# Optimization experiments

Measured on AMD Instinct MI355X. Metric: run time of the kernel, lower is better.

## Reference

```python
import jax, jax.numpy as jnp
import numpy as np

D = 300      # embedding / model dim
H = 150      # LSTM hidden per direction (dim // 2)
V = 21257    # vocab size
B, S = 1024, 256


def _lstm_run(x, lengths, Wih, Whh, b):
    """Unidirectional masked LSTM. x: [B,S,Din]; outputs [B,S,H].
    State frozen and output zeroed at t >= lengths (packed-sequence semantics)."""
    Bb, Ss, _ = x.shape
    h0 = jnp.zeros((Bb, H), x.dtype)
    c0 = jnp.zeros((Bb, H), x.dtype)

    def step(carry, inp):
        h, c = carry
        xt, t = inp
        g = xt @ Wih.T + h @ Whh.T + b          # [B, 4H]
        i, f, gg, o = jnp.split(g, 4, axis=-1)   # torch gate order i,f,g,o
        i = jax.nn.sigmoid(i); f = jax.nn.sigmoid(f)
        gg = jnp.tanh(gg); o = jax.nn.sigmoid(o)
        c_new = f * c + i * gg
        h_new = o * jnp.tanh(c_new)
        valid = (t < lengths)[:, None]
        h2 = jnp.where(valid, h_new, h)
        c2 = jnp.where(valid, c_new, c)
        return (h2, c2), jnp.where(valid, h_new, jnp.zeros_like(h_new))

    _, ys = jax.lax.scan(step, (h0, c0), (jnp.swapaxes(x, 0, 1), jnp.arange(Ss)))
    return jnp.swapaxes(ys, 0, 1)


def _reverse_valid(x, lengths):
    """Reverse the valid prefix of each sequence; self-inverse on valid region."""
    Ss = x.shape[1]
    t = jnp.arange(Ss)[None, :]
    L = lengths[:, None]
    idx = jnp.where(t < L, L - 1 - t, t)
    return jnp.take_along_axis(x, idx[:, :, None], axis=1)


def _bilstm(x, lengths, pf, pb):
    hf = _lstm_run(x, lengths, *pf)
    hb = _reverse_valid(_lstm_run(_reverse_valid(x, lengths), lengths, *pb), lengths)
    return jnp.concatenate([hf, hb], axis=-1)  # [B,S,2H]


def setup_inputs() -> dict:
    key = jax.random.key(0)
    ks = jax.random.split(key, 20)
    x = jax.random.randint(ks[0], (B, S), 0, V)
    lengths = jax.random.randint(ks[1], (B,), 1, S + 1)
    mask = (jnp.arange(S)[None, :] < lengths[:, None]).astype(jnp.int64)

    def p(k, shape):
        return jax.random.normal(k, shape, dtype=jnp.float32) * 0.05

    emb = p(ks[2], (V, D))
    inp = {"x": x, "mask": mask, "emb": emb}
    # layer 0: input D; layer 1: input 2H (=D)
    names = [("l0f", D), ("l0b", D), ("l1f", 2 * H), ("l1b", 2 * H)]
    ki = 3
    for nm, din in names:
        inp[f"Wih_{nm}"] = p(ks[ki], (4 * H, din)); ki += 1
        inp[f"Whh_{nm}"] = p(ks[ki], (4 * H, H)); ki += 1
        inp[f"b_{nm}"] = p(ks[ki], (4 * H,)); ki += 1
    inp["W1"] = p(ks[15], (D, D)); inp["b1"] = p(ks[16], (D,))
    inp["W2"] = p(ks[17], (D, D)); inp["b2"] = p(ks[18], (D,))
    return inp


def reference(x, mask, emb,
              Wih_l0f, Whh_l0f, b_l0f, Wih_l0b, Whh_l0b, b_l0b,
              Wih_l1f, Whh_l1f, b_l1f, Wih_l1b, Whh_l1b, b_l1b,
              W1, b1, W2, b2):
    lengths = jnp.sum(mask != 0, axis=1)
    emb_z = emb.at[0].set(0.0)                 # padding_idx=0
    xe = emb_z[x]                              # [B,S,D]
    h1 = _bilstm(xe, lengths, (Wih_l0f, Whh_l0f, b_l0f), (Wih_l0b, Whh_l0b, b_l0b))
    h2 = _bilstm(h1, lengths, (Wih_l1f, Whh_l1f, b_l1f), (Wih_l1b, Whh_l1b, b_l1b))
    # gather output at last valid timestep (fwd last step || bwd first step)
    last = jnp.take_along_axis(h2, (lengths - 1)[:, None, None], axis=1)[:, 0, :]  # [B,300]
    # dropout is identity in eval mode
    out = jnp.tanh(last @ W1.T + b1)
    out = out @ W2.T + b2
    return out
```

## Files before the change

kernel.cpp:

```cpp
#include <hip/hip_runtime.h>

typedef unsigned short u16;
typedef __bf16 bf16x8 __attribute__((ext_vector_type(8)));
typedef float f32x4 __attribute__((ext_vector_type(4)));
typedef float f4 __attribute__((ext_vector_type(4)));
typedef unsigned short u16x8 __attribute__((ext_vector_type(8)));
typedef unsigned short u16x4 __attribute__((ext_vector_type(4)));

#define BB 1024
#define SS 256
#define DD 300
#define HH 150
#define GG 600
#define VV 21257
#define VPAD 21376
#define KSTR 320
#define GSTR 600
#define WK 160
#define L2E 1.442695041f
#define L2E2 2.885390082f

static __device__ __forceinline__ float bf2f(u16 u){
  unsigned v = ((unsigned)u) << 16;
  return __builtin_bit_cast(float, v);
}
static __device__ __forceinline__ u16 f2bf(float f){
  unsigned u = __builtin_bit_cast(unsigned, f);
  u = u + 0x7FFFu + ((u >> 16) & 1u);
  return (u16)(u >> 16);
}
static __device__ __forceinline__ float fsig2(float p){
  return __builtin_amdgcn_rcpf(1.0f + __builtin_amdgcn_exp2f(-p));
}
static __device__ __forceinline__ float ftanh2(float p){
  return 2.0f * __builtin_amdgcn_rcpf(1.0f + __builtin_amdgcn_exp2f(-p)) - 1.0f;
}

__global__ void k_len(const int* __restrict__ mask, int* __restrict__ len){
  __shared__ int red[256];
  int b = blockIdx.x, t = threadIdx.x;
  red[t] = (mask[b*SS + t] != 0) ? 1 : 0;
  __syncthreads();
  for (int o = 128; o > 0; o >>= 1){
    if (t < o) red[t] += red[t+o];
    __syncthreads();
  }
  if (t == 0) len[b] = red[0];
}

__global__ void k_sort(const int* __restrict__ len, int* __restrict__ perm){
  __shared__ int L[1024];
  int b = threadIdx.x;
  int l = len[b];
  L[b] = l;
  __syncthreads();
  int r = 0;
  for (int j = 0; j < 1024; ++j){
    int lj = L[j];
    r += (lj < l) || (lj == l && j < b);
  }
  perm[r] = b;
}

struct PrepW {
  const float* src[8];
  u16* dst[8];
  int R[8], C[8], DR[8], DC[8];
};
__global__ void k_prepw(PrepW p){
  int z = blockIdx.y;
  int n = p.DR[z]*p.DC[z];
  for (int i = blockIdx.x*256 + threadIdx.x; i < n; i += 800*256){
    int r = i / p.DC[z], c = i - r*p.DC[z];
    float v = (r < p.R[z] && c < p.C[z]) ? p.src[z][r*p.C[z] + c] : 0.f;
    float sc = (r >= 300 && r < 450) ? L2E2 : L2E;
    p.dst[z][i] = f2bf(v * sc);
  }
}
struct PrepB { const float* src[4]; float* dst[4]; };
__global__ void k_prepb(PrepB p){
  int z = blockIdx.y;
  int i = blockIdx.x*256 + threadIdx.x;
  if (i < 640){
    float v = (i < GG) ? p.src[z][i] : 0.f;
    float sc = (i >= 300 && i < 450) ? L2E2 : L2E;
    p.dst[z][i] = v * sc;
  }
}

__global__ void k_prepemb(const float* __restrict__ emb, u16* __restrict__ dst){
  long i = (long)blockIdx.x*256 + threadIdx.x;
  if (i >= (long)VPAD*KSTR) return;
  int r = (int)(i / KSTR), c = (int)(i - (long)r*KSTR);
  float v = (r >= 1 && r < VV && c < DD) ? emb[(size_t)r*DD + c] : 0.f;
  dst[i] = f2bf(v);
}

__launch_bounds__(512, 2)
__global__ void k_gemm(const u16* __restrict__ A,
                       const u16* __restrict__ Wf, const u16* __restrict__ Wb,
                       const float* __restrict__ bsf, const float* __restrict__ bsb,
                       u16* __restrict__ of, u16* __restrict__ ob)
{
  const u16* W = blockIdx.z ? Wb : Wf;
  const float* bias = blockIdx.z ? bsb : bsf;
  u16* outp = blockIdx.z ? ob : of;

  __shared__ u16 Al[128*40];
  __shared__ u16 Bl[320*40];

  int tid = threadIdx.x;
  int l = tid & 63, w = tid >> 6;
  int lo = l & 15, hi = l >> 4;
  int wm = w >> 2, wn = w & 3;
  int m0 = blockIdx.x * 128;
  int n0 = blockIdx.y * 320;

  int ar = tid >> 2, ac = (tid & 3) * 8;
  const u16* Arow = A + (size_t)(m0 + ar)*KSTR + ac;
  bool bvld[3]; int brr[3], bcc[3];
  const u16* Brow[3];
  #pragma unroll
  for (int i = 0; i < 3; ++i){
    int ch = tid + i*512;
    bvld[i] = (ch < 1280);
    int r2 = bvld[i] ? (ch >> 2) : 0;
    brr[i] = r2; bcc[i] = (ch & 3) * 8;
    Brow[i] = W + (size_t)(n0 + r2)*KSTR + bcc[i];
  }

  u16x8 ra = *(const u16x8*)Arow;
  u16x8 rbv[3];
  #pragma unroll
  for (int i = 0; i < 3; ++i) if (bvld[i]) rbv[i] = *(const u16x8*)Brow[i];

  f32x4 zero = {0.f, 0.f, 0.f, 0.f};
  f32x4 acc[4][5];
  #pragma unroll
  for (int a = 0; a < 4; ++a)
    #pragma unroll
    for (int b = 0; b < 5; ++b) acc[a][b] = zero;

  for (int kk = 0; kk < 10; ++kk){
    __syncthreads();
    *(u16x8*)&Al[ar*40 + ac] = ra;
    #pragma unroll
    for (int i = 0; i < 3; ++i)
      if (bvld[i]) *(u16x8*)&Bl[brr[i]*40 + bcc[i]] = rbv[i];
    __syncthreads();
    if (kk < 9){
      int k1 = (kk+1)*32;
      ra = *(const u16x8*)(Arow + k1);
      #pragma unroll
      for (int i = 0; i < 3; ++i)
        if (bvld[i]) rbv[i] = *(const u16x8*)(Brow[i] + k1);
    }
    u16x8 av[4], bv[5];
    #pragma unroll
    for (int mt = 0; mt < 4; ++mt)
      av[mt] = *(const u16x8*)&Al[(wm*64 + mt*16 + lo)*40 + hi*8];
    #pragma unroll
    for (int nt = 0; nt < 5; ++nt)
      bv[nt] = *(const u16x8*)&Bl[(wn*80 + nt*16 + lo)*40 + hi*8];
    #pragma unroll
    for (int mt = 0; mt < 4; ++mt)
      #pragma unroll
      for (int nt = 0; nt < 5; ++nt)
        acc[mt][nt] = __builtin_amdgcn_mfma_f32_16x16x32_bf16(
            __builtin_bit_cast(bf16x8, av[mt]),
            __builtin_bit_cast(bf16x8, bv[nt]),
            acc[mt][nt], 0, 0, 0);
  }

  #pragma unroll
  for (int mt = 0; mt < 4; ++mt){
    #pragma unroll
    for (int nt = 0; nt < 5; ++nt){
      int col = n0 + wn*80 + nt*16 + lo;
      if (col < GG){
        float bsv = bias[col];
        int g = (col >= 450) ? 3 : (col >= 300) ? 2 : (col >= 150) ? 1 : 0;
        int cofs = (col - g*150)*4 + g;
        #pragma unroll
        for (int r = 0; r < 4; ++r){
          int row = m0 + wm*64 + mt*16 + hi*4 + r;
          outp[(size_t)row*GSTR + cofs] = f2bf(acc[mt][nt][r] + bsv);
        }
      }
    }
  }
}

#define PREF(GB, TT)                                                            \
  {                                                                             \
    _Pragma("unroll")                                                           \
    for (int r = 0; r < 4; ++r){                                                \
      int Li = Lr[r];                                                           \
      int tt = ((TT) < Li) ? (TT) : (Li-1);                                     \
      int s_ = dir ? (Li-1-tt) : tt;                                            \
      int rowi;                                                                 \
      if (isL1) rowi = rowb[r] + s_;                                            \
      else      rowi = (int)tks[(hi*4+r)*256 + s_];                             \
      GB[r] = *(const u16x4*)(xg + (size_t)rowi*GSTR + jjc*4);                  \
    }                                                                           \
  }

#define REC_STEP(T, PB, GB)                                                     \
  {                                                                             \
    f32x4 acc0 = {0,0,0,0}, acc1 = {0,0,0,0}, acc2 = {0,0,0,0}, acc3 = {0,0,0,0}; \
    _Pragma("unroll")                                                           \
    for (int ks = 0; ks < 5; ++ks){                                             \
      u16x8 a_ = *(const u16x8*)&hsm[PB][lo*168 + ks*32 + hi*8];                \
      acc0 = __builtin_amdgcn_mfma_f32_16x16x32_bf16(                           \
          __builtin_bit_cast(bf16x8, a_), __builtin_bit_cast(bf16x8, bw[0][ks]), acc0, 0,0,0); \
      acc1 = __builtin_amdgcn_mfma_f32_16x16x32_bf16(                           \
          __builtin_bit_cast(bf16x8, a_), __builtin_bit_cast(bf16x8, bw[1][ks]), acc1, 0,0,0); \
      acc2 = __builtin_amdgcn_mfma_f32_16x16x32_bf16(                           \
          __builtin_bit_cast(bf16x8, a_), __builtin_bit_cast(bf16x8, bw[2][ks]), acc2, 0,0,0); \
      acc3 = __builtin_amdgcn_mfma_f32_16x16x32_bf16(                           \
          __builtin_bit_cast(bf16x8, a_), __builtin_bit_cast(bf16x8, bw[3][ks]), acc3, 0,0,0); \
    }                                                                           \
    _Pragma("unroll")                                                           \
    for (int r = 0; r < 4; ++r){                                                \
      if (jv && (T) < Lr[r]){                                                   \
        float pi = acc0[r] + bf2f(GB[r][0]);                                    \
        float pf = acc1[r] + bf2f(GB[r][1]);                                    \
        float pg = acc2[r] + bf2f(GB[r][2]);                                    \
        float po = acc3[r] + bf2f(GB[r][3]);                                    \
        float ig = fsig2(pi), fg = fsig2(pf), g2 = ftanh2(pg), og = fsig2(po);  \
        float cc = fg*cst[r] + ig*g2;  cst[r] = cc;                             \
        float hn = og * ftanh2(L2E2 * cc);                                      \
        u16 hb = f2bf(hn);                                                      \
        hsm[(PB)^1][(hi*4+r)*168 + jj] = hb;                                    \
        if (!isL1){                                                             \
          int s_ = dir ? (Lr[r]-1-(T)) : (T);                                   \
          h1[(size_t)(rowb[r]+s_)*KSTR + dir*150 + jj] = hb;                    \
        } else {                                                                \
          bool isl = dir ? ((T)==0) : ((T)==Lr[r]-1);                           \
          if (isl) lastf[(size_t)bo2[r]*304 + dir*150 + jj] = hn;               \
        }                                                                       \
      }                                                                         \
    }                                                                           \
    if ((T)+4 < maxL){                                                          \
      PREF(GB, (T)+4)                                                           \
    }                                                                           \
    __builtin_amdgcn_sched_barrier(0);                                          \
    asm volatile("s_waitcnt lgkmcnt(0)" ::: "memory");                          \
    __builtin_amdgcn_s_barrier();                                               \
    __builtin_amdgcn_sched_barrier(0);                                          \
  }

__launch_bounds__(640, 2)
__global__ void k_recM(const u16* __restrict__ gF, const u16* __restrict__ gBf,
                       const u16* __restrict__ tF, const u16* __restrict__ tB,
                       const u16* __restrict__ Wh0F, const u16* __restrict__ Wh0B,
                       const u16* __restrict__ Wh1F, const u16* __restrict__ Wh1B,
                       const int* __restrict__ len, const int* __restrict__ perm,
                       const int* __restrict__ x,
                       u16* __restrict__ h1, float* __restrict__ lastf,
                       int coA, int coB, int mode0)
{
  const int isL1 = (blockIdx.z == 0) ? mode0 : 0;
  const int dir  = blockIdx.y;
  const int tile = blockIdx.x;
  const int co   = isL1 ? coA : coB;
  const u16* xg  = isL1 ? (dir ? gBf : gF) : (dir ? tB : tF);
  const u16* Whh = isL1 ? (dir ? Wh1B : Wh1F) : (dir ? Wh0B : Wh0F);

  __shared__ u16 hsm[2][16*168];
  __shared__ u16 tks[16*256];
  __shared__ int Ls[16], rbL[16], boS[16];

  int tid = threadIdx.x;
  int l = tid & 63, w = tid >> 6;
  int lo = l & 15, hi = l >> 4;
  int jj = w*16 + lo;
  bool jv = (jj < HH);
  int jjc = jv ? jj : 0;

  u16x8 bw[4][5];
  #pragma unroll
  for (int g = 0; g < 4; ++g)
    #pragma unroll
    for (int ks = 0; ks < 5; ++ks)
      bw[g][ks] = *(const u16x8*)(Whh + (size_t)(g*150 + jj)*WK + ks*32 + hi*8);

  for (int i = tid; i < 2*16*168; i += 640) ((u16*)hsm)[i] = 0;
  if (tid < 16){
    int b = perm[co + tile*16 + tid];
    Ls[tid]  = len[b];
    rbL[tid] = (tile*16 + tid)*SS;
    boS[tid] = b;
  }
  __syncthreads();
  if (!isL1){
    for (int idx = tid; idx < 16*256; idx += 640){
      int i = idx >> 8, s = idx & 255;
      tks[idx] = (u16)x[boS[i]*SS + s];
    }
  }
  __syncthreads();

  int maxL = Ls[15];
  int Lr[4], rowb[4], bo2[4];
  #pragma unroll
  for (int r = 0; r < 4; ++r){
    int i = hi*4 + r;
    Lr[r] = Ls[i]; rowb[r] = rbL[i]; bo2[r] = boS[i];
  }

  float cst[4] = {0.f, 0.f, 0.f, 0.f};
  u16x4 g0[4], g1[4], g2b[4], g3[4];
  PREF(g0, 0)
  PREF(g1, 1)
  PREF(g2b, 2)
  PREF(g3, 3)

  for (int t = 0; t < maxL; t += 4){
    REC_STEP(t, 0, g0)
    if (t + 1 < maxL) REC_STEP(t+1, 1, g1)
    if (t + 2 < maxL) REC_STEP(t+2, 0, g2b)
    if (t + 3 < maxL) REC_STEP(t+3, 1, g3)
  }
}

__global__ void k_cls(const float* __restrict__ lastf,
                      const float* __restrict__ W1, const float* __restrict__ b1,
                      const float* __restrict__ W2, const float* __restrict__ b2,
                      float* __restrict__ out)
{
  __shared__ float inb[8][304];
  __shared__ float mid[8][304];
  int r0 = blockIdx.x * 8, tid = threadIdx.x;
  for (int i = tid; i < 8*76; i += 256){
    int r = i / 76, c4 = i - r*76;
    ((f4*)&inb[r][0])[c4] = ((const f4*)(lastf + (size_t)(r0+r)*304))[c4];
  }
  __syncthreads();
  for (int item = tid; item < 2400; item += 256){
    int r = item / 300, c = item - r*300;
    const f4* wr = (const f4*)(W1 + (size_t)c*300);
    const f4* xr = (const f4*)&inb[r][0];
    f4 a0 = {0,0,0,0}, a1 = {0,0,0,0}, a2 = {0,0,0,0};
    for (int k = 0; k < 75; k += 3){
      a0 += xr[k]   * wr[k];
      a1 += xr[k+1] * wr[k+1];
      a2 += xr[k+2] * wr[k+2];
    }
    f4 s4 = a0 + a1 + a2;
    float a = s4[0] + s4[1] + s4[2] + s4[3] + b1[c];
    mid[r][c] = 2.0f * __builtin_amdgcn_rcpf(1.0f + __builtin_amdgcn_exp2f(-L2E2*a)) - 1.0f;
  }
  __syncthreads();
  for (int item = tid; item < 2400; item += 256){
    int r = item / 300, c = item - r*300;
    const f4* wr = (const f4*)(W2 + (size_t)c*300);
    const f4* xr = (const f4*)&mid[r][0];
    f4 a0 = {0,0,0,0}, a1 = {0,0,0,0}, a2 = {0,0,0,0};
    for (int k = 0; k < 75; k += 3){
      a0 += xr[k]   * wr[k];
      a1 += xr[k+1] * wr[k+1];
      a2 += xr[k+2] * wr[k+2];
    }
    f4 s4 = a0 + a1 + a2;
    out[(size_t)(r0+r)*300 + c] = s4[0] + s4[1] + s4[2] + s4[3] + b2[c];
  }
}

extern "C" void kernel_launch(void* const* d_in, const int* in_sizes, int n_in,
                              void* d_out, int out_size, void* d_ws, size_t ws_size,
                              hipStream_t stream)
{
  const int*   x    = (const int*)d_in[0];
  const int*   mask = (const int*)d_in[1];
  const float* emb  = (const float*)d_in[2];
  const float* Wih[4] = {(const float*)d_in[3], (const float*)d_in[6],
                         (const float*)d_in[9], (const float*)d_in[12]};
  const float* Whh[4] = {(const float*)d_in[4], (const float*)d_in[7],
                         (const float*)d_in[10], (const float*)d_in[13]};
  const float* bs[4]  = {(const float*)d_in[5], (const float*)d_in[8],
                         (const float*)d_in[11], (const float*)d_in[14]};
  const float* W1 = (const float*)d_in[15];
  const float* b1 = (const float*)d_in[16];
  const float* W2 = (const float*)d_in[17];
  const float* b2 = (const float*)d_in[18];
  float* out = (float*)d_out;

  char* p = (char*)d_ws;
  auto alloc = [&](size_t bytes){ char* r = p; p += (bytes + 255) & ~(size_t)255; return r; };

  u16 *WihP[4], *WhhP[4];
  for (int i = 0; i < 4; ++i){
    WihP[i] = (u16*)alloc(640*320*2);
    WhhP[i] = (u16*)alloc(640*160*2);
  }
  float* biasP[4];
  for (int i = 0; i < 4; ++i) biasP[i] = (float*)alloc(640*4);
  int* len  = (int*)alloc(1024*4);
  int* perm = (int*)alloc(1024*4);
  float* lastf = (float*)alloc((size_t)1024*304*4);
  u16* embP = (u16*)alloc((size_t)VPAD*KSTR*2);
  u16* tabF = (u16*)alloc((size_t)VPAD*GSTR*2);
  u16* tabB = (u16*)alloc((size_t)VPAD*GSTR*2);
  size_t fixed_end = (size_t)(p - (char*)d_ws);

  const size_t per_sample = (size_t)SS*KSTR*2 + 2*(size_t)SS*GSTR*2;
  int nc = 32;
  const int cands[6] = {1, 2, 4, 8, 16, 32};
  for (int ci = 0; ci < 6; ++ci){
    size_t need = fixed_end + (size_t)(BB / cands[ci]) * per_sample + (1u<<20);
    if (need <= ws_size){ nc = cands[ci]; break; }
  }
  const int Bc = BB / nc;
  const int Mc = Bc * SS;

  u16* h1    = (u16*)alloc((size_t)Mc*KSTR*2);
  u16* gateF = (u16*)alloc((size_t)Mc*GSTR*2);
  u16* gateB = (u16*)alloc((size_t)Mc*GSTR*2);

  hipMemsetAsync(h1, 0, (size_t)Mc*KSTR*2, stream);

  k_len <<<dim3(1024), dim3(256), 0, stream>>>(mask, len);
  k_sort<<<dim3(1),    dim3(1024),0, stream>>>(len, perm);

  PrepW pw;
  for (int i = 0; i < 4; ++i){
    pw.src[i] = Wih[i]; pw.dst[i] = WihP[i];
    pw.R[i] = GG; pw.C[i] = DD; pw.DR[i] = 640; pw.DC[i] = KSTR;
    pw.src[4+i] = Whh[i]; pw.dst[4+i] = WhhP[i];
    pw.R[4+i] = GG; pw.C[4+i] = HH; pw.DR[4+i] = 640; pw.DC[4+i] = WK;
  }
  k_prepw<<<dim3(800, 8), dim3(256), 0, stream>>>(pw);

  PrepB pb;
  for (int i = 0; i < 4; ++i){ pb.src[i] = bs[i]; pb.dst[i] = biasP[i]; }
  k_prepb<<<dim3(3, 4), dim3(256), 0, stream>>>(pb);

  k_prepemb<<<dim3((VPAD*KSTR + 255)/256), dim3(256), 0, stream>>>(emb, embP);

  k_gemm<<<dim3(VPAD/128, 2, 2), dim3(512), 0, stream>>>(embP, WihP[0], WihP[1],
                                                         biasP[0], biasP[1], tabF, tabB);

  k_recM<<<dim3(Bc/16, 2, 1), dim3(640), 0, stream>>>(gateF, gateB, tabF, tabB,
                                                      WhhP[0], WhhP[1], WhhP[2], WhhP[3],
                                                      len, perm, x, h1, lastf,
                                                      0, 0, 0);
  k_gemm<<<dim3(Mc/128, 2, 2), dim3(512), 0, stream>>>(h1, WihP[2], WihP[3],
                                                       biasP[2], biasP[3], gateF, gateB);
  for (int c = 0; c < nc; ++c){
    if (c + 1 < nc){
      k_recM<<<dim3(Bc/16, 2, 2), dim3(640), 0, stream>>>(gateF, gateB, tabF, tabB,
                                                          WhhP[0], WhhP[1], WhhP[2], WhhP[3],
                                                          len, perm, x, h1, lastf,
                                                          c*Bc, (c+1)*Bc, 1);
      k_gemm<<<dim3(Mc/128, 2, 2), dim3(512), 0, stream>>>(h1, WihP[2], WihP[3],
                                                           biasP[2], biasP[3], gateF, gateB);
    } else {
      k_recM<<<dim3(Bc/16, 2, 1), dim3(640), 0, stream>>>(gateF, gateB, tabF, tabB,
                                                          WhhP[0], WhhP[1], WhhP[2], WhhP[3],
                                                          len, perm, x, h1, lastf,
                                                          c*Bc, 0, 1);
    }
  }

  k_cls<<<dim3(128), dim3(256), 0, stream>>>(lastf, W1, b1, W2, b2, out);
}
```

Before: 3.483 ms.

## Process two batch tiles per recurrent block and load GEMM operands directly from global

The recurrent kernel now handles two 16-row batch tiles per workgroup, interleaving their MFMA chains and gate math between barriers. This halves the grid and amortizes the register-resident Whh weights and per-step barrier across twice the work, giving more independent work per sync. The input GEMM drops its LDS staging and loads MFMA fragments straight from global memory with register double buffering, removing the __syncthreads. In exchange the recurrent kernel needs more registers and has fewer blocks, so fewer CUs may be busy, and the GEMM now reads the same operands from global once per wave.

```diff
diff --git a/kernel.cpp b/kernel.cpp
--- a/kernel.cpp
+++ b/kernel.cpp
@@ -106,9 +106,6 @@
   const float* bias = blockIdx.z ? bsb : bsf;
   u16* outp = blockIdx.z ? ob : of;
 
-  __shared__ u16 Al[128*40];
-  __shared__ u16 Bl[320*40];
-
   int tid = threadIdx.x;
   int l = tid & 63, w = tid >> 6;
   int lo = l & 15, hi = l >> 4;
@@ -116,23 +113,14 @@
   int m0 = blockIdx.x * 128;
   int n0 = blockIdx.y * 320;
 
-  int ar = tid >> 2, ac = (tid & 3) * 8;
-  const u16* Arow = A + (size_t)(m0 + ar)*KSTR + ac;
-  bool bvld[3]; int brr[3], bcc[3];
-  const u16* Brow[3];
-  #pragma unroll
-  for (int i = 0; i < 3; ++i){
-    int ch = tid + i*512;
-    bvld[i] = (ch < 1280);
-    int r2 = bvld[i] ? (ch >> 2) : 0;
-    brr[i] = r2; bcc[i] = (ch & 3) * 8;
-    Brow[i] = W + (size_t)(n0 + r2)*KSTR + bcc[i];
-  }
-
-  u16x8 ra = *(const u16x8*)Arow;
-  u16x8 rbv[3];
-  #pragma unroll
-  for (int i = 0; i < 3; ++i) if (bvld[i]) rbv[i] = *(const u16x8*)Brow[i];
+  const u16* Abase = A + (size_t)(m0 + wm*64 + lo)*KSTR + hi*8;
+  const u16* Bbase = W + (size_t)(n0 + wn*80 + lo)*KSTR + hi*8;
+
+  u16x8 avA[4], bvA[5], avB[4], bvB[5];
+  #pragma unroll
+  for (int mt = 0; mt < 4; ++mt) avA[mt] = *(const u16x8*)(Abase + (size_t)mt*16*KSTR);
+  #pragma unroll
+  for (int nt = 0; nt < 5; ++nt) bvA[nt] = *(const u16x8*)(Bbase + (size_t)nt*16*KSTR);
 
   f32x4 zero = {0.f, 0.f, 0.f, 0.f};
   f32x4 acc[4][5];
@@ -141,34 +129,36 @@
     #pragma unroll
     for (int b = 0; b < 5; ++b) acc[a][b] = zero;
 
-  for (int kk = 0; kk < 10; ++kk){
-    __syncthreads();
-    *(u16x8*)&Al[ar*40 + ac] = ra;
-    #pragma unroll
-    for (int i = 0; i < 3; ++i)
-      if (bvld[i]) *(u16x8*)&Bl[brr[i]*40 + bcc[i]] = rbv[i];
-    __syncthreads();
-    if (kk < 9){
-      int k1 = (kk+1)*32;
-      ra = *(const u16x8*)(Arow + k1);
-      #pragma unroll
-      for (int i = 0; i < 3; ++i)
-        if (bvld[i]) rbv[i] = *(const u16x8*)(Brow[i] + k1);
-    }
-    u16x8 av[4], bv[5];
-    #pragma unroll
-    for (int mt = 0; mt < 4; ++mt)
-      av[mt] = *(const u16x8*)&Al[(wm*64 + mt*16 + lo)*40 + hi*8];
-    #pragma unroll
-    for (int nt = 0; nt < 5; ++nt)
-      bv[nt] = *(const u16x8*)&Bl[(wn*80 + nt*16 + lo)*40 + hi*8];
+  for (int kk = 0; kk < 10; kk += 2){
+    {
+      int kc = (kk+1)*32;
+      #pragma unroll
+      for (int mt = 0; mt < 4; ++mt) avB[mt] = *(const u16x8*)(Abase + (size_t)mt*16*KSTR + kc);
+      #pragma unroll
+      for (int nt = 0; nt < 5; ++nt) bvB[nt] = *(const u16x8*)(Bbase + (size_t)nt*16*KSTR + kc);
+    }
     #pragma unroll
     for (int mt = 0; mt < 4; ++mt)
       #pragma unroll
       for (int nt = 0; nt < 5; ++nt)
         acc[mt][nt] = __builtin_amdgcn_mfma_f32_16x16x32_bf16(
-            __builtin_bit_cast(bf16x8, av[mt]),
-            __builtin_bit_cast(bf16x8, bv[nt]),
+            __builtin_bit_cast(bf16x8, avA[mt]),
+            __builtin_bit_cast(bf16x8, bvA[nt]),
+            acc[mt][nt], 0, 0, 0);
+    if (kk + 2 < 10){
+      int kc = (kk+2)*32;
+      #pragma unroll
+      for (int mt = 0; mt < 4; ++mt) avA[mt] = *(const u16x8*)(Abase + (size_t)mt*16*KSTR + kc);
+      #pragma unroll
+      for (int nt = 0; nt < 5; ++nt) bvA[nt] = *(const u16x8*)(Bbase + (size_t)nt*16*KSTR + kc);
+    }
+    #pragma unroll
+    for (int mt = 0; mt < 4; ++mt)
+      #pragma unroll
+      for (int nt = 0; nt < 5; ++nt)
+        acc[mt][nt] = __builtin_amdgcn_mfma_f32_16x16x32_bf16(
+            __builtin_bit_cast(bf16x8, avB[mt]),
+            __builtin_bit_cast(bf16x8, bvB[nt]),
             acc[mt][nt], 0, 0, 0);
   }
 
@@ -191,65 +181,6 @@
   }
 }
 
-#define PREF(GB, TT)                                                            \
-  {                                                                             \
-    _Pragma("unroll")                                                           \
-    for (int r = 0; r < 4; ++r){                                                \
-      int Li = Lr[r];                                                           \
-      int tt = ((TT) < Li) ? (TT) : (Li-1);                                     \
-      int s_ = dir ? (Li-1-tt) : tt;                                            \
-      int rowi;                                                                 \
-      if (isL1) rowi = rowb[r] + s_;                                            \
-      else      rowi = (int)tks[(hi*4+r)*256 + s_];                             \
-      GB[r] = *(const u16x4*)(xg + (size_t)rowi*GSTR + jjc*4);                  \
-    }                                                                           \
-  }
-
-#define REC_STEP(T, PB, GB)                                                     \
-  {                                                                             \
-    f32x4 acc0 = {0,0,0,0}, acc1 = {0,0,0,0}, acc2 = {0,0,0,0}, acc3 = {0,0,0,0}; \
-    _Pragma("unroll")                                                           \
-    for (int ks = 0; ks < 5; ++ks){                                             \
-      u16x8 a_ = *(const u16x8*)&hsm[PB][lo*168 + ks*32 + hi*8];                \
-      acc0 = __builtin_amdgcn_mfma_f32_16x16x32_bf16(                           \
-          __builtin_bit_cast(bf16x8, a_), __builtin_bit_cast(bf16x8, bw[0][ks]), acc0, 0,0,0); \
-      acc1 = __builtin_amdgcn_mfma_f32_16x16x32_bf16(                           \
-          __builtin_bit_cast(bf16x8, a_), __builtin_bit_cast(bf16x8, bw[1][ks]), acc1, 0,0,0); \
-      acc2 = __builtin_amdgcn_mfma_f32_16x16x32_bf16(                           \
-          __builtin_bit_cast(bf16x8, a_), __builtin_bit_cast(bf16x8, bw[2][ks]), acc2, 0,0,0); \
-      acc3 = __builtin_amdgcn_mfma_f32_16x16x32_bf16(                           \
-          __builtin_bit_cast(bf16x8, a_), __builtin_bit_cast(bf16x8, bw[3][ks]), acc3, 0,0,0); \
-    }                                                                           \
-    _Pragma("unroll")                                                           \
-    for (int r = 0; r < 4; ++r){                                                \
-      if (jv && (T) < Lr[r]){                                                   \
-        float pi = acc0[r] + bf2f(GB[r][0]);                                    \
-        float pf = acc1[r] + bf2f(GB[r][1]);                                    \
-        float pg = acc2[r] + bf2f(GB[r][2]);                                    \
-        float po = acc3[r] + bf2f(GB[r][3]);                                    \
-        float ig = fsig2(pi), fg = fsig2(pf), g2 = ftanh2(pg), og = fsig2(po);  \
-        float cc = fg*cst[r] + ig*g2;  cst[r] = cc;                             \
-        float hn = og * ftanh2(L2E2 * cc);                                      \
-        u16 hb = f2bf(hn);                                                      \
-        hsm[(PB)^1][(hi*4+r)*168 + jj] = hb;                                    \
-        if (!isL1){                                                             \
-          int s_ = dir ? (Lr[r]-1-(T)) : (T);                                   \
-          h1[(size_t)(rowb[r]+s_)*KSTR + dir*150 + jj] = hb;                    \
-        } else {                                                                \
-          bool isl = dir ? ((T)==0) : ((T)==Lr[r]-1);                           \
-          if (isl) lastf[(size_t)bo2[r]*304 + dir*150 + jj] = hn;               \
-        }                                                                       \
-      }                                                                         \
-    }                                                                           \
-    if ((T)+4 < maxL){                                                          \
-      PREF(GB, (T)+4)                                                           \
-    }                                                                           \
-    __builtin_amdgcn_sched_barrier(0);                                          \
-    asm volatile("s_waitcnt lgkmcnt(0)" ::: "memory");                          \
-    __builtin_amdgcn_s_barrier();                                               \
-    __builtin_amdgcn_sched_barrier(0);                                          \
-  }
-
 __launch_bounds__(640, 2)
 __global__ void k_recM(const u16* __restrict__ gF, const u16* __restrict__ gBf,
                        const u16* __restrict__ tF, const u16* __restrict__ tB,
@@ -262,14 +193,14 @@
 {
   const int isL1 = (blockIdx.z == 0) ? mode0 : 0;
   const int dir  = blockIdx.y;
-  const int tile = blockIdx.x;
+  const int pr   = blockIdx.x;
   const int co   = isL1 ? coA : coB;
   const u16* xg  = isL1 ? (dir ? gBf : gF) : (dir ? tB : tF);
   const u16* Whh = isL1 ? (dir ? Wh1B : Wh1F) : (dir ? Wh0B : Wh0F);
 
-  __shared__ u16 hsm[2][16*168];
-  __shared__ u16 tks[16*256];
-  __shared__ int Ls[16], rbL[16], boS[16];
+  __shared__ u16 hsm[2][2][16*168];
+  __shared__ u16 tks[2][16*256];
+  __shared__ int Ls[2][16], rbL[2][16], boS[2][16];
 
   int tid = threadIdx.x;
   int l = tid & 63, w = tid >> 6;
@@ -285,42 +216,102 @@
     for (int ks = 0; ks < 5; ++ks)
       bw[g][ks] = *(const u16x8*)(Whh + (size_t)(g*150 + jj)*WK + ks*32 + hi*8);
 
-  for (int i = tid; i < 2*16*168; i += 640) ((u16*)hsm)[i] = 0;
-  if (tid < 16){
-    int b = perm[co + tile*16 + tid];
-    Ls[tid]  = len[b];
-    rbL[tid] = (tile*16 + tid)*SS;
-    boS[tid] = b;
+  for (int i = tid; i < 2*2*16*168; i += 640) ((u16*)hsm)[i] = 0;
+  if (tid < 32){
+    int tl = tid >> 4, i = tid & 15;
+    int b = perm[co + (pr*2 + tl)*16 + i];
+    Ls[tl][i]  = len[b];
+    rbL[tl][i] = ((pr*2 + tl)*16 + i)*SS;
+    boS[tl][i] = b;
   }
   __syncthreads();
   if (!isL1){
-    for (int idx = tid; idx < 16*256; idx += 640){
-      int i = idx >> 8, s = idx & 255;
-      tks[idx] = (u16)x[boS[i]*SS + s];
-    }
-  }
-  __syncthreads();
-
-  int maxL = Ls[15];
-  int Lr[4], rowb[4], bo2[4];
-  #pragma unroll
-  for (int r = 0; r < 4; ++r){
-    int i = hi*4 + r;
-    Lr[r] = Ls[i]; rowb[r] = rbL[i]; bo2[r] = boS[i];
-  }
-
-  float cst[4] = {0.f, 0.f, 0.f, 0.f};
-  u16x4 g0[4], g1[4], g2b[4], g3[4];
-  PREF(g0, 0)
-  PREF(g1, 1)
-  PREF(g2b, 2)
-  PREF(g3, 3)
-
-  for (int t = 0; t < maxL; t += 4){
-    REC_STEP(t, 0, g0)
-    if (t + 1 < maxL) REC_STEP(t+1, 1, g1)
-    if (t + 2 < maxL) REC_STEP(t+2, 0, g2b)
-    if (t + 3 < maxL) REC_STEP(t+3, 1, g3)
+    for (int idx = tid; idx < 2*16*256; idx += 640){
+      int tl = idx >> 12, rest = idx & 4095;
+      int i = rest >> 8, s = rest & 255;
+      tks[tl][i*256 + s] = (u16)x[boS[tl][i]*SS + s];
+    }
+  }
+  __syncthreads();
+
+  int maxL = Ls[1][15];
+  int Lr[2][4], rowb[2][4], bo2[2][4];
+  #pragma unroll
+  for (int tl = 0; tl < 2; ++tl)
+    #pragma unroll
+    for (int r = 0; r < 4; ++r){
+      int i = hi*4 + r;
+      Lr[tl][r] = Ls[tl][i]; rowb[tl][r] = rbL[tl][i]; bo2[tl][r] = boS[tl][i];
+    }
+
+  float cst[2][4] = {{0.f,0.f,0.f,0.f},{0.f,0.f,0.f,0.f}};
+  u16x4 gA[2][4], gB[2][4];
+
+  auto pref = [&](int tl, u16x4 (&G)[4], int TT){
+    #pragma unroll
+    for (int r = 0; r < 4; ++r){
+      int Li = Lr[tl][r];
+      int tt = (TT < Li) ? TT : (Li-1);
+      int s_ = dir ? (Li-1-tt) : tt;
+      int rowi = isL1 ? (rowb[tl][r] + s_) : (int)tks[tl][(hi*4+r)*256 + s_];
+      G[r] = *(const u16x4*)(xg + (size_t)rowi*GSTR + jjc*4);
+    }
+  };
+
+  auto recstep = [&](int T, int PB, u16x4 (&GBB)[2][4]){
+    f32x4 acc[2][4];
+    #pragma unroll
+    for (int tl = 0; tl < 2; ++tl){
+      #pragma unroll
+      for (int g = 0; g < 4; ++g) acc[tl][g] = (f32x4){0.f,0.f,0.f,0.f};
+      #pragma unroll
+      for (int ks = 0; ks < 5; ++ks){
+        u16x8 a_ = *(const u16x8*)&hsm[tl][PB][lo*168 + ks*32 + hi*8];
+        #pragma unroll
+        for (int g = 0; g < 4; ++g)
+          acc[tl][g] = __builtin_amdgcn_mfma_f32_16x16x32_bf16(
+              __builtin_bit_cast(bf16x8, a_),
+              __builtin_bit_cast(bf16x8, bw[g][ks]),
+              acc[tl][g], 0, 0, 0);
+      }
+    }
+    #pragma unroll
+    for (int tl = 0; tl < 2; ++tl){
+      #pragma unroll
+      for (int r = 0; r < 4; ++r){
+        if (jv && T < Lr[tl][r]){
+          float pi = acc[tl][0][r] + bf2f(GBB[tl][r][0]);
+          float pf = acc[tl][1][r] + bf2f(GBB[tl][r][1]);
+          float pg = acc[tl][2][r] + bf2f(GBB[tl][r][2]);
+          float po = acc[tl][3][r] + bf2f(GBB[tl][r][3]);
+          float ig = fsig2(pi), fg = fsig2(pf), g2 = ftanh2(pg), og = fsig2(po);
+          float cc = fg*cst[tl][r] + ig*g2;  cst[tl][r] = cc;
+          float hn = og * ftanh2(L2E2 * cc);
+          u16 hb = f2bf(hn);
+          hsm[tl][PB^1][(hi*4+r)*168 + jj] = hb;
+          if (!isL1){
+            int s_ = dir ? (Lr[tl][r]-1-T) : T;
+            h1[(size_t)(rowb[tl][r]+s_)*KSTR + dir*150 + jj] = hb;
+          } else {
+            bool isl = dir ? (T == 0) : (T == Lr[tl][r]-1);
+            if (isl) lastf[(size_t)bo2[tl][r]*304 + dir*150 + jj] = hn;
+          }
+        }
+      }
+      if (T + 2 < maxL) pref(tl, GBB[tl], T + 2);
+    }
+    __builtin_amdgcn_sched_barrier(0);
+    asm volatile("s_waitcnt lgkmcnt(0)" ::: "memory");
+    __builtin_amdgcn_s_barrier();
+    __builtin_amdgcn_sched_barrier(0);
+  };
+
+  pref(0, gA[0], 0); pref(1, gA[1], 0);
+  pref(0, gB[0], 1); pref(1, gB[1], 1);
+
+  for (int t = 0; t < maxL; t += 2){
+    recstep(t, 0, gA);
+    if (t + 1 < maxL) recstep(t+1, 1, gB);
   }
 }
 
@@ -441,7 +432,7 @@
   k_gemm<<<dim3(VPAD/128, 2, 2), dim3(512), 0, stream>>>(embP, WihP[0], WihP[1],
                                                          biasP[0], biasP[1], tabF, tabB);
 
-  k_recM<<<dim3(Bc/16, 2, 1), dim3(640), 0, stream>>>(gateF, gateB, tabF, tabB,
+  k_recM<<<dim3(Bc/32, 2, 1), dim3(640), 0, stream>>>(gateF, gateB, tabF, tabB,
                                                       WhhP[0], WhhP[1], WhhP[2], WhhP[3],
                                                       len, perm, x, h1, lastf,
                                                       0, 0, 0);
@@ -449,14 +440,14 @@
                                                        biasP[2], biasP[3], gateF, gateB);
   for (int c = 0; c < nc; ++c){
     if (c + 1 < nc){
-      k_recM<<<dim3(Bc/16, 2, 2), dim3(640), 0, stream>>>(gateF, gateB, tabF, tabB,
+      k_recM<<<dim3(Bc/32, 2, 2), dim3(640), 0, stream>>>(gateF, gateB, tabF, tabB,
                                                           WhhP[0], WhhP[1], WhhP[2], WhhP[3],
                                                           len, perm, x, h1, lastf,
                                                           c*Bc, (c+1)*Bc, 1);
       k_gemm<<<dim3(Mc/128, 2, 2), dim3(512), 0, stream>>>(h1, WihP[2], WihP[3],
                                                            biasP[2], biasP[3], gateF, gateB);
     } else {
-      k_recM<<<dim3(Bc/16, 2, 1), dim3(640), 0, stream>>>(gateF, gateB, tabF, tabB,
+      k_recM<<<dim3(Bc/32, 2, 1), dim3(640), 0, stream>>>(gateF, gateB, tabF, tabB,
                                                           WhhP[0], WhhP[1], WhhP[2], WhhP[3],
                                                           len, perm, x, h1, lastf,
                                                           c*Bc, 0, 1);
```

Result: slower. 10.76 ms (+208.9%).

## Stage recurrent h outputs in LDS and drop LDS staging in gate GEMM

Applied to the files above, without the earlier changes.

The recurrent kernel now buffers four timesteps of layer-0 hidden outputs in a double-buffered shared-memory page and flushes them as 16-byte vector stores. This replaces the scattered 2-byte global stores made on every step. To keep those stores aligned, the backward half of h1 moves to column offset 160, and the layer-1 input weights are remapped so their columns skip the 10-column gap. Separately, the gate GEMM drops its LDS tiles and barriers and loads MFMA operands straight from global memory into registers with double buffering, which trades shared-memory traffic for more redundant global/L2 reads.

```diff
diff --git a/kernel.cpp b/kernel.cpp
--- a/kernel.cpp
+++ b/kernel.cpp
@@ -65,14 +65,21 @@
 struct PrepW {
   const float* src[8];
   u16* dst[8];
-  int R[8], C[8], DR[8], DC[8];
+  int R[8], C[8], DR[8], DC[8], RM[8];
 };
 __global__ void k_prepw(PrepW p){
   int z = blockIdx.y;
   int n = p.DR[z]*p.DC[z];
   for (int i = blockIdx.x*256 + threadIdx.x; i < n; i += 800*256){
     int r = i / p.DC[z], c = i - r*p.DC[z];
-    float v = (r < p.R[z] && c < p.C[z]) ? p.src[z][r*p.C[z] + c] : 0.f;
+    int cs = c; bool ok = true;
+    if (p.RM[z]){
+      if (c < 150)      cs = c;
+      else if (c < 160) ok = false;
+      else if (c < 310) cs = c - 10;
+      else              ok = false;
+    }
+    float v = (ok && r < p.R[z] && cs < p.C[z]) ? p.src[z][r*p.C[z] + cs] : 0.f;
     float sc = (r >= 300 && r < 450) ? L2E2 : L2E;
     p.dst[z][i] = f2bf(v * sc);
   }
@@ -106,9 +113,6 @@
   const float* bias = blockIdx.z ? bsb : bsf;
   u16* outp = blockIdx.z ? ob : of;
 
-  __shared__ u16 Al[128*40];
-  __shared__ u16 Bl[320*40];
-
   int tid = threadIdx.x;
   int l = tid & 63, w = tid >> 6;
   int lo = l & 15, hi = l >> 4;
@@ -116,59 +120,51 @@
   int m0 = blockIdx.x * 128;
   int n0 = blockIdx.y * 320;
 
-  int ar = tid >> 2, ac = (tid & 3) * 8;
-  const u16* Arow = A + (size_t)(m0 + ar)*KSTR + ac;
-  bool bvld[3]; int brr[3], bcc[3];
-  const u16* Brow[3];
-  #pragma unroll
-  for (int i = 0; i < 3; ++i){
-    int ch = tid + i*512;
-    bvld[i] = (ch < 1280);
-    int r2 = bvld[i] ? (ch >> 2) : 0;
-    brr[i] = r2; bcc[i] = (ch & 3) * 8;
-    Brow[i] = W + (size_t)(n0 + r2)*KSTR + bcc[i];
-  }
-
-  u16x8 ra = *(const u16x8*)Arow;
-  u16x8 rbv[3];
-  #pragma unroll
-  for (int i = 0; i < 3; ++i) if (bvld[i]) rbv[i] = *(const u16x8*)Brow[i];
-
-  f32x4 zero = {0.f, 0.f, 0.f, 0.f};
+  const u16* Abase = A + (size_t)(m0 + wm*64 + lo)*KSTR + hi*8;
+  const u16* Bbase = W + (size_t)(n0 + wn*80 + lo)*KSTR + hi*8;
+
+  u16x8 avA[4], bvA[5], avB[4], bvB[5];
+  #pragma unroll
+  for (int mt = 0; mt < 4; ++mt) avA[mt] = *(const u16x8*)(Abase + (size_t)mt*16*KSTR);
+  #pragma unroll
+  for (int nt = 0; nt < 5; ++nt) bvA[nt] = *(const u16x8*)(Bbase + (size_t)nt*16*KSTR);
+
   f32x4 acc[4][5];
   #pragma unroll
   for (int a = 0; a < 4; ++a)
     #pragma unroll
-    for (int b = 0; b < 5; ++b) acc[a][b] = zero;
-
-  for (int kk = 0; kk < 10; ++kk){
-    __syncthreads();
-    *(u16x8*)&Al[ar*40 + ac] = ra;
-    #pragma unroll
-    for (int i = 0; i < 3; ++i)
-      if (bvld[i]) *(u16x8*)&Bl[brr[i]*40 + bcc[i]] = rbv[i];
-    __syncthreads();
-    if (kk < 9){
-      int k1 = (kk+1)*32;
-      ra = *(const u16x8*)(Arow + k1);
-      #pragma unroll
-      for (int i = 0; i < 3; ++i)
-        if (bvld[i]) rbv[i] = *(const u16x8*)(Brow[i] + k1);
-    }
-    u16x8 av[4], bv[5];
+    for (int b = 0; b < 5; ++b) acc[a][b] = (f32x4){0.f,0.f,0.f,0.f};
+
+  for (int kk = 0; kk < 10; kk += 2){
+    {
+      int kc = (kk+1)*32;
+      #pragma unroll
+      for (int mt = 0; mt < 4; ++mt) avB[mt] = *(const u16x8*)(Abase + (size_t)mt*16*KSTR + kc);
+      #pragma unroll
+      for (int nt = 0; nt < 5; ++nt) bvB[nt] = *(const u16x8*)(Bbase + (size_t)nt*16*KSTR + kc);
+    }
     #pragma unroll
     for (int mt = 0; mt < 4; ++mt)
-      av[mt] = *(const u16x8*)&Al[(wm*64 + mt*16 + lo)*40 + hi*8];
-    #pragma unroll
-    for (int nt = 0; nt < 5; ++nt)
-      bv[nt] = *(const u16x8*)&Bl[(wn*80 + nt*16 + lo)*40 + hi*8];
+      #pragma unroll
+      for (int nt = 0; nt < 5; ++nt)
+        acc[mt][nt] = __builtin_amdgcn_mfma_f32_16x16x32_bf16(
+            __builtin_bit_cast(bf16x8, avA[mt]),
+            __builtin_bit_cast(bf16x8, bvA[nt]),
+            acc[mt][nt], 0, 0, 0);
+    if (kk + 2 < 10){
+      int kc = (kk+2)*32;
+      #pragma unroll
+      for (int mt = 0; mt < 4; ++mt) avA[mt] = *(const u16x8*)(Abase + (size_t)mt*16*KSTR + kc);
+      #pragma unroll
+      for (int nt = 0; nt < 5; ++nt) bvA[nt] = *(const u16x8*)(Bbase + (size_t)nt*16*KSTR + kc);
+    }
     #pragma unroll
     for (int mt = 0; mt < 4; ++mt)
       #pragma unroll
       for (int nt = 0; nt < 5; ++nt)
         acc[mt][nt] = __builtin_amdgcn_mfma_f32_16x16x32_bf16(
-            __builtin_bit_cast(bf16x8, av[mt]),
-            __builtin_bit_cast(bf16x8, bv[nt]),
+            __builtin_bit_cast(bf16x8, avB[mt]),
+            __builtin_bit_cast(bf16x8, bvB[nt]),
             acc[mt][nt], 0, 0, 0);
   }
 
@@ -205,7 +201,7 @@
     }                                                                           \
   }
 
-#define REC_STEP(T, PB, GB)                                                     \
+#define REC_STEP(T, PB, GB, Q, PG)                                              \
   {                                                                             \
     f32x4 acc0 = {0,0,0,0}, acc1 = {0,0,0,0}, acc2 = {0,0,0,0}, acc3 = {0,0,0,0}; \
     _Pragma("unroll")                                                           \
@@ -223,18 +219,17 @@
     _Pragma("unroll")                                                           \
     for (int r = 0; r < 4; ++r){                                                \
       if (jv && (T) < Lr[r]){                                                   \
-        float pi = acc0[r] + bf2f(GB[r][0]);                                    \
-        float pf = acc1[r] + bf2f(GB[r][1]);                                    \
-        float pg = acc2[r] + bf2f(GB[r][2]);                                    \
-        float po = acc3[r] + bf2f(GB[r][3]);                                    \
-        float ig = fsig2(pi), fg = fsig2(pf), g2 = ftanh2(pg), og = fsig2(po);  \
+        float pi  = acc0[r] + bf2f(GB[r][0]);                                   \
+        float pf  = acc1[r] + bf2f(GB[r][1]);                                   \
+        float pgv = acc2[r] + bf2f(GB[r][2]);                                   \
+        float po  = acc3[r] + bf2f(GB[r][3]);                                   \
+        float ig = fsig2(pi), fg = fsig2(pf), g2 = ftanh2(pgv), og = fsig2(po); \
         float cc = fg*cst[r] + ig*g2;  cst[r] = cc;                             \
         float hn = og * ftanh2(L2E2 * cc);                                      \
         u16 hb = f2bf(hn);                                                      \
         hsm[(PB)^1][(hi*4+r)*168 + jj] = hb;                                    \
         if (!isL1){                                                             \
-          int s_ = dir ? (Lr[r]-1-(T)) : (T);                                   \
-          h1[(size_t)(rowb[r]+s_)*KSTR + dir*150 + jj] = hb;                    \
+          hout[PG][hi*4+r][Q][jj] = hb;                                         \
         } else {                                                                \
           bool isl = dir ? ((T)==0) : ((T)==Lr[r]-1);                           \
           if (isl) lastf[(size_t)bo2[r]*304 + dir*150 + jj] = hn;               \
@@ -248,6 +243,24 @@
     asm volatile("s_waitcnt lgkmcnt(0)" ::: "memory");                          \
     __builtin_amdgcn_s_barrier();                                               \
     __builtin_amdgcn_sched_barrier(0);                                          \
+  }
+
+#define FLUSH(TB, PBF)                                                          \
+  if (!isL1){                                                                   \
+    _Pragma("unroll")                                                           \
+    for (int pass = 0; pass < 2; ++pass){                                       \
+      int task = tid + pass*640;                                                \
+      if (task < 1216){                                                         \
+        int i = task / 76; int rem = task - i*76;                               \
+        int q = rem / 19;  int c8 = (rem - q*19)*8;                             \
+        int Li = Ls[i]; int tt = (TB) + q;                                      \
+        if (tt < Li && tt < maxL){                                              \
+          int s_ = dir ? (Li-1-tt) : tt;                                        \
+          *(u16x8*)(h1 + (size_t)(rbL[i]+s_)*KSTR + dir*160 + c8) =             \
+              *(const u16x8*)&hout[PBF][i][q][c8];                              \
+        }                                                                       \
+      }                                                                         \
+    }                                                                           \
   }
 
 __launch_bounds__(640, 2)
@@ -268,6 +281,7 @@
   const u16* Whh = isL1 ? (dir ? Wh1B : Wh1F) : (dir ? Wh0B : Wh0F);
 
   __shared__ u16 hsm[2][16*168];
+  __shared__ u16 hout[2][16][4][152];
   __shared__ u16 tks[16*256];
   __shared__ int Ls[16], rbL[16], boS[16];
 
@@ -286,6 +300,7 @@
       bw[g][ks] = *(const u16x8*)(Whh + (size_t)(g*150 + jj)*WK + ks*32 + hi*8);
 
   for (int i = tid; i < 2*16*168; i += 640) ((u16*)hsm)[i] = 0;
+  for (int i = tid; i < 2*16*4*152; i += 640) ((u16*)hout)[i] = 0;
   if (tid < 16){
     int b = perm[co + tile*16 + tid];
     Ls[tid]  = len[b];
@@ -317,10 +332,24 @@
   PREF(g3, 3)
 
   for (int t = 0; t < maxL; t += 4){
-    REC_STEP(t, 0, g0)
-    if (t + 1 < maxL) REC_STEP(t+1, 1, g1)
-    if (t + 2 < maxL) REC_STEP(t+2, 0, g2b)
-    if (t + 3 < maxL) REC_STEP(t+3, 1, g3)
+    int page = (t >> 2) & 1;
+    if (t >= 4){ FLUSH(t-4, page^1) }
+    if (page == 0){
+      REC_STEP(t, 0, g0, 0, 0)
+      if (t + 1 < maxL) REC_STEP(t+1, 1, g1, 1, 0)
+      if (t + 2 < maxL) REC_STEP(t+2, 0, g2b, 2, 0)
+      if (t + 3 < maxL) REC_STEP(t+3, 1, g3, 3, 0)
+    } else {
+      REC_STEP(t, 0, g0, 0, 1)
+      if (t + 1 < maxL) REC_STEP(t+1, 1, g1, 1, 1)
+      if (t + 2 < maxL) REC_STEP(t+2, 0, g2b, 2, 1)
+      if (t + 3 < maxL) REC_STEP(t+3, 1, g3, 3, 1)
+    }
+  }
+  {
+    int lastg = ((maxL-1) >> 2) << 2;
+    int pbl   = ((maxL-1) >> 2) & 1;
+    FLUSH(lastg, pbl)
   }
 }
 
@@ -418,7 +447,7 @@
   u16* gateF = (u16*)alloc((size_t)Mc*GSTR*2);
   u16* gateB = (u16*)alloc((size_t)Mc*GSTR*2);
 
-  hipMemsetAsync(h1, 0, (size_t)Mc*KSTR*2, stream);
+  (void)hipMemsetAsync(h1, 0, (size_t)Mc*KSTR*2, stream);
 
   k_len <<<dim3(1024), dim3(256), 0, stream>>>(mask, len);
   k_sort<<<dim3(1),    dim3(1024),0, stream>>>(len, perm);
@@ -426,9 +455,11 @@
   PrepW pw;
   for (int i = 0; i < 4; ++i){
     pw.src[i] = Wih[i]; pw.dst[i] = WihP[i];
-    pw.R[i] = GG; pw.C[i] = DD; pw.DR[i] = 640; pw.DC[i] = KSTR;
+    pw.R[i] = GG; pw.C[i] = (i < 2) ? DD : 2*HH; pw.DR[i] = 640; pw.DC[i] = KSTR;
+    pw.RM[i] = (i >= 2) ? 1 : 0;
     pw.src[4+i] = Whh[i]; pw.dst[4+i] = WhhP[i];
     pw.R[4+i] = GG; pw.C[4+i] = HH; pw.DR[4+i] = 640; pw.DC[4+i] = WK;
+    pw.RM[4+i] = 0;
   }
   k_prepw<<<dim3(800, 8), dim3(256), 0, stream>>>(pw);
 
```

Result: slower. 5.945 ms (+70.7%).
